# Performance work log

Measured on AMD Instinct MI355X. Metric: run time of the kernel, lower is better.

## Reference

```python
import jax, jax.numpy as jnp
import numpy as np

# hyperparams from __init__
K_SEL = 8          # SoftSelectorProxy K
R_TEMP = 1.0       # SoftSelectorProxy r (temperature)
LAM = 0.5          # SoftSelectorProxy lam (blend)
MAX_PROXY = 16     # max_proxy_points -> K_eff (N >> 16)

B, N, INPUT_DIM = 32, 16384, 64
HID, K_DIM, D_MODEL = 64, 16, 512
ANCHOR_DIM = INPUT_DIM + 2  # structural_feature_dim: x feats + saliency + normalized position


def setup_inputs() -> dict:
    key = jax.random.key(0)
    ks = jax.random.split(key, 10)
    s = lambda k, shp, fan: jax.random.normal(k, shp, jnp.float32) * (1.0 / np.sqrt(fan))
    return {
        "x": jax.random.normal(ks[0], (B, N, INPUT_DIM), jnp.float32),
        "W1": s(ks[1], (INPUT_DIM, HID), INPUT_DIM),
        "b1": jnp.zeros((HID,), jnp.float32),
        "w_e": s(ks[2], (HID,), HID),
        "w_s": s(ks[3], (HID,), HID),
        "W_lift": s(ks[4], (ANCHOR_DIM, K_DIM), ANCHOR_DIM),
        "b_lift": jnp.zeros((K_DIM,), jnp.float32),
        "W_proj": s(ks[5], (K_DIM, D_MODEL), K_DIM),
        "b_proj": jnp.zeros((D_MODEL,), jnp.float32),
        "mu": jnp.zeros((ANCHOR_DIM,), jnp.float32),
        "sigma": jnp.ones((ANCHOR_DIM,), jnp.float32),
    }


def reference(x, W1, b1, w_e, w_s, W_lift, b_lift, W_proj, b_proj, mu, sigma):
    # CausalEventModel: shared hidden, event + saliency heads
    h = jnp.tanh(jnp.einsum('bnd,dh->bnh', x, W1) + b1)          # [B,N,HID]
    saliency = jax.nn.softplus(jnp.einsum('bnh,h->bn', h, w_s))   # [B,N]
    # SoftSelectorProxy: blend of sigmoid gate and K-scaled softmax (soft top-K relaxation)
    y_star = LAM * jax.nn.sigmoid(saliency / R_TEMP) + (1.0 - LAM) * K_SEL * jax.nn.softmax(saliency / R_TEMP, axis=1)  # [B,N]
    # dense_anchor_vectors: concat features, saliency, normalized position
    pos = jnp.broadcast_to((jnp.arange(N, dtype=jnp.float32) / N)[None, :, None], (x.shape[0], N, 1))
    dense = jnp.concatenate([x, saliency[..., None], pos], axis=-1)  # [B,N,ANCHOR_DIM]
    # NormalizedLift: normalize then linear lift to k_dim
    lifted = jnp.einsum('bna,ak->bnk', (dense - mu) / sigma, W_lift) + b_lift  # [B,N,K_DIM]
    # topk selection + gather + projection
    _, top_idx = jax.lax.top_k(y_star, MAX_PROXY)                 # [B,MAX_PROXY]
    cloud = jnp.take_along_axis(lifted, top_idx[..., None], axis=1)  # [B,MAX_PROXY,K_DIM]
    tokens = jnp.einsum('bkc,cd->bkd', cloud, W_proj) + b_proj    # [B,MAX_PROXY,D_MODEL]
    return tokens, y_star
```

## Files before the change

kernel.cpp:

```cpp
#include <hip/hip_runtime.h>
#include <math.h>

#define B 32
#define N 16384
#define DIM 64
#define HID 64
#define KD 16
#define DM 512
#define MP 16

#define GRID_SAL 1024
#define ITERS 8

typedef __attribute__((ext_vector_type(8))) _Float16 f16x8;
typedef __attribute__((ext_vector_type(2))) __fp16 fph2;
typedef __attribute__((ext_vector_type(4))) float f32x4;

__device__ __forceinline__ float fast_tanh(float a) {
  const float e = __expf(2.f * a);
  return 1.f - 2.f * __builtin_amdgcn_rcpf(e + 1.f);
}

__global__ __launch_bounds__(256) void k_prepw(
    const float* __restrict__ W1, _Float16* __restrict__ Wt_hi, _Float16* __restrict__ Wt_lo) {
  const int i = blockIdx.x * 256 + threadIdx.x;
  const int col = i >> 6, k = i & 63;
  const float v = W1[k * HID + col];
  const _Float16 h = (_Float16)v;
  Wt_hi[i] = h;
  Wt_lo[i] = (_Float16)(v - (float)h);
}

__global__ __launch_bounds__(256) void k_saliency(
    const float* __restrict__ x, const _Float16* __restrict__ Wt_hi,
    const _Float16* __restrict__ Wt_lo, const float* __restrict__ b1,
    const float* __restrict__ w_s, float* __restrict__ sal) {
  const int t = threadIdx.x;
  const int lane = t & 63, wid = t >> 6;
  const int c16 = lane & 15, kq = lane >> 4;
  const int wbase = c16 * 64 + kq * 8;

  f16x8 WH[8], WL[8];
#pragma unroll
  for (int ct = 0; ct < 4; ++ct)
#pragma unroll
    for (int kc = 0; kc < 2; ++kc) {
      const int off = ct * 1024 + kc * 32 + wbase;
      WH[ct * 2 + kc] = *(const f16x8*)(Wt_hi + off);
      WL[ct * 2 + kc] = *(const f16x8*)(Wt_lo + off);
    }

#define PKSPLIT(va, vb, HW, LW) {                                                  \
    const fph2 h_ = __builtin_amdgcn_cvt_pkrtz((va), (vb));                        \
    const fph2 l_ = __builtin_amdgcn_cvt_pkrtz((va) - (float)h_[0],                \
                                               (vb) - (float)h_[1]);               \
    HW = __builtin_bit_cast(unsigned, h_);                                         \
    LW = __builtin_bit_cast(unsigned, l_); }

#define SAL_LOADS(b0, b1_, b2, b3, it_) {                                          \
    const size_t row_ = ((size_t)(it_) * GRID_SAL + blockIdx.x) * 64 + wid * 16 + c16; \
    const float* __restrict__ p_ = x + row_ * DIM + kq * 8;                        \
    b0 = *(const float4*)(p_);       b1_ = *(const float4*)(p_ + 4);               \
    b2 = *(const float4*)(p_ + 32);  b3 = *(const float4*)(p_ + 36); }

#define SAL_COMPUTE(b0, b1_, b2, b3, it_) {                                        \
    f32x4 a0 = (f32x4)0.f, a1 = (f32x4)0.f, a2 = (f32x4)0.f, a3 = (f32x4)0.f;      \
    {                                                                  \
      uint4 H, L;                                                                  \
      PKSPLIT(b0.x, b0.y, H.x, L.x); PKSPLIT(b0.z, b0.w, H.y, L.y);                \
      PKSPLIT(b1_.x, b1_.y, H.z, L.z); PKSPLIT(b1_.z, b1_.w, H.w, L.w);            \
      const f16x8 bh = __builtin_bit_cast(f16x8, H);                               \
      const f16x8 bl = __builtin_bit_cast(f16x8, L);                               \
      a0 = __builtin_amdgcn_mfma_f32_16x16x32_f16(WH[0], bh, a0, 0, 0, 0);         \
      a1 = __builtin_amdgcn_mfma_f32_16x16x32_f16(WH[2], bh, a1, 0, 0, 0);         \
      a2 = __builtin_amdgcn_mfma_f32_16x16x32_f16(WH[4], bh, a2, 0, 0, 0);         \
      a3 = __builtin_amdgcn_mfma_f32_16x16x32_f16(WH[6], bh, a3, 0, 0, 0);         \
      a0 = __builtin_amdgcn_mfma_f32_16x16x32_f16(WL[0], bh, a0, 0, 0, 0);         \
      a1 = __builtin_amdgcn_mfma_f32_16x16x32_f16(WL[2], bh, a1, 0, 0, 0);         \
      a2 = __builtin_amdgcn_mfma_f32_16x16x32_f16(WL[4], bh, a2, 0, 0, 0);         \
      a3 = __builtin_amdgcn_mfma_f32_16x16x32_f16(WL[6], bh, a3, 0, 0, 0);         \
      a0 = __builtin_amdgcn_mfma_f32_16x16x32_f16(WH[0], bl, a0, 0, 0, 0);         \
      a1 = __builtin_amdgcn_mfma_f32_16x16x32_f16(WH[2], bl, a1, 0, 0, 0);         \
      a2 = __builtin_amdgcn_mfma_f32_16x16x32_f16(WH[4], bl, a2, 0, 0, 0);         \
      a3 = __builtin_amdgcn_mfma_f32_16x16x32_f16(WH[6], bl, a3, 0, 0, 0);         \
    }                                                                              \
    {                                                                  \
      uint4 H, L;                                                                  \
      PKSPLIT(b2.x, b2.y, H.x, L.x); PKSPLIT(b2.z, b2.w, H.y, L.y);                \
      PKSPLIT(b3.x, b3.y, H.z, L.z); PKSPLIT(b3.z, b3.w, H.w, L.w);                \
      const f16x8 bh = __builtin_bit_cast(f16x8, H);                               \
      const f16x8 bl = __builtin_bit_cast(f16x8, L);                               \
      a0 = __builtin_amdgcn_mfma_f32_16x16x32_f16(WH[1], bh, a0, 0, 0, 0);         \
      a1 = __builtin_amdgcn_mfma_f32_16x16x32_f16(WH[3], bh, a1, 0, 0, 0);         \
      a2 = __builtin_amdgcn_mfma_f32_16x16x32_f16(WH[5], bh, a2, 0, 0, 0);         \
      a3 = __builtin_amdgcn_mfma_f32_16x16x32_f16(WH[7], bh, a3, 0, 0, 0);         \
      a0 = __builtin_amdgcn_mfma_f32_16x16x32_f16(WL[1], bh, a0, 0, 0, 0);         \
      a1 = __builtin_amdgcn_mfma_f32_16x16x32_f16(WL[3], bh, a1, 0, 0, 0);         \
      a2 = __builtin_amdgcn_mfma_f32_16x16x32_f16(WL[5], bh, a2, 0, 0, 0);         \
      a3 = __builtin_amdgcn_mfma_f32_16x16x32_f16(WL[7], bh, a3, 0, 0, 0);         \
      a0 = __builtin_amdgcn_mfma_f32_16x16x32_f16(WH[1], bl, a0, 0, 0, 0);         \
      a1 = __builtin_amdgcn_mfma_f32_16x16x32_f16(WH[3], bl, a1, 0, 0, 0);         \
      a2 = __builtin_amdgcn_mfma_f32_16x16x32_f16(WH[5], bl, a2, 0, 0, 0);         \
      a3 = __builtin_amdgcn_mfma_f32_16x16x32_f16(WH[7], bl, a3, 0, 0, 0);         \
    }                                                                              \
       \
    float s = 0.f;                                                                 \
    { const f32x4 wv = *(const f32x4*)(w_s + kq * 4);                              \
      const f32x4 bv = *(const f32x4*)(b1 + kq * 4);                               \
      s = fmaf(wv[0], fast_tanh(a0[0] + bv[0]), s);                                \
      s = fmaf(wv[1], fast_tanh(a0[1] + bv[1]), s);                                \
      s = fmaf(wv[2], fast_tanh(a0[2] + bv[2]), s);                                \
      s = fmaf(wv[3], fast_tanh(a0[3] + bv[3]), s); }                              \
    { const f32x4 wv = *(const f32x4*)(w_s + 16 + kq * 4);                         \
      const f32x4 bv = *(const f32x4*)(b1 + 16 + kq * 4);                          \
      s = fmaf(wv[0], fast_tanh(a1[0] + bv[0]), s);                                \
      s = fmaf(wv[1], fast_tanh(a1[1] + bv[1]), s);                                \
      s = fmaf(wv[2], fast_tanh(a1[2] + bv[2]), s);                                \
      s = fmaf(wv[3], fast_tanh(a1[3] + bv[3]), s); }                              \
    { const f32x4 wv = *(const f32x4*)(w_s + 32 + kq * 4);                         \
      const f32x4 bv = *(const f32x4*)(b1 + 32 + kq * 4);                          \
      s = fmaf(wv[0], fast_tanh(a2[0] + bv[0]), s);                                \
      s = fmaf(wv[1], fast_tanh(a2[1] + bv[1]), s);                                \
      s = fmaf(wv[2], fast_tanh(a2[2] + bv[2]), s);                                \
      s = fmaf(wv[3], fast_tanh(a2[3] + bv[3]), s); }                              \
    { const f32x4 wv = *(const f32x4*)(w_s + 48 + kq * 4);                         \
      const f32x4 bv = *(const f32x4*)(b1 + 48 + kq * 4);                          \
      s = fmaf(wv[0], fast_tanh(a3[0] + bv[0]), s);                                \
      s = fmaf(wv[1], fast_tanh(a3[1] + bv[1]), s);                                \
      s = fmaf(wv[2], fast_tanh(a3[2] + bv[2]), s);                                \
      s = fmaf(wv[3], fast_tanh(a3[3] + bv[3]), s); }                              \
    s += __shfl_xor(s, 16);                                                        \
    s += __shfl_xor(s, 32);                                                        \
    if (lane < 16) {                                                               \
      const size_t sr_ = ((size_t)(it_) * GRID_SAL + blockIdx.x) * 64 + wid * 16 + lane; \
      const float z_ = __expf(-fabsf(s));                                          \
      sal[sr_] = fmaxf(s, 0.f) + __logf(1.f + z_);          \
    } }

  float4 pA0, pA1, pA2, pA3;
  float4 pB0, pB1, pB2, pB3;

  SAL_LOADS(pA0, pA1, pA2, pA3, 0);
#pragma unroll 1
  for (int it2 = 0; it2 < ITERS; it2 += 2) {
    SAL_LOADS(pB0, pB1, pB2, pB3, it2 + 1);
    SAL_COMPUTE(pA0, pA1, pA2, pA3, it2);
    if (it2 + 2 < ITERS) SAL_LOADS(pA0, pA1, pA2, pA3, it2 + 2);
    SAL_COMPUTE(pB0, pB1, pB2, pB3, it2 + 1);
  }
#undef SAL_LOADS
#undef SAL_COMPUTE
#undef PKSPLIT
}

__global__ __launch_bounds__(256) void k_chunk(
    const float* __restrict__ sal, float* __restrict__ cmax, float* __restrict__ csum,
    float* __restrict__ cval, int* __restrict__ cidx) {
  __shared__ float sb[4], ss[4], wv[4];
  __shared__ int wi[4];
  const int t = threadIdx.x, c = blockIdx.x;
  const int rowoff = (c & 7) * 2048;
  const size_t gbase = (size_t)c * 2048;
  float v[8];
#pragma unroll
  for (int j = 0; j < 8; ++j) v[j] = sal[gbase + t + 256 * j];

  float m = v[0];
#pragma unroll
  for (int j = 1; j < 8; ++j) m = fmaxf(m, v[j]);
#pragma unroll
  for (int off = 1; off < 64; off <<= 1) m = fmaxf(m, __shfl_xor(m, off));
  if ((t & 63) == 0) sb[t >> 6] = m;
  __syncthreads();
  m = fmaxf(fmaxf(sb[0], sb[1]), fmaxf(sb[2], sb[3]));

  float se = 0.f;
#pragma unroll
  for (int j = 0; j < 8; ++j) se += __expf(v[j] - m);
#pragma unroll
  for (int off = 1; off < 64; off <<= 1) se += __shfl_xor(se, off);
  if ((t & 63) == 0) ss[t >> 6] = se;
  __syncthreads();
  if (t == 0) { cmax[c] = m; csum[c] = ss[0] + ss[1] + ss[2] + ss[3]; }

  for (int k = 0; k < MP; ++k) {
    float bv = v[0]; int bj = 0;
#pragma unroll
    for (int j = 1; j < 8; ++j)
      if (v[j] > bv) { bv = v[j]; bj = j; }
    int bi = rowoff + t + 256 * bj;
#pragma unroll
    for (int off = 1; off < 64; off <<= 1) {
      const float ov = __shfl_xor(bv, off);
      const int   oi = __shfl_xor(bi, off);
      if (ov > bv || (ov == bv && oi < bi)) { bv = ov; bi = oi; }
    }
    if ((t & 63) == 0) { wv[t >> 6] = bv; wi[t >> 6] = bi; }
    __syncthreads();
    float Bv = wv[0]; int Bi = wi[0];
#pragma unroll
    for (int w = 1; w < 4; ++w)
      if (wv[w] > Bv || (wv[w] == Bv && wi[w] < Bi)) { Bv = wv[w]; Bi = wi[w]; }
    if (t == 0) { cval[c * MP + k] = Bv; cidx[c * MP + k] = Bi; }
    const int relidx = Bi - rowoff;
#pragma unroll
    for (int jj = 0; jj < 8; ++jj)
      if (relidx == t + 256 * jj) v[jj] = -INFINITY;
    __syncthreads();
  }
}

__global__ __launch_bounds__(256) void k_ystar(
    float* __restrict__ y, const float* __restrict__ cmax, const float* __restrict__ csum) {
  const int b = blockIdx.x >> 6;
  const int gi = blockIdx.x * 256 + threadIdx.x;
  float mx = cmax[b * 8];
#pragma unroll
  for (int c = 1; c < 8; ++c) mx = fmaxf(mx, cmax[b * 8 + c]);
  float S = 0.f;
#pragma unroll
  for (int c = 0; c < 8; ++c) S += csum[b * 8 + c] * __expf(cmax[b * 8 + c] - mx);
  const float inv = __builtin_amdgcn_rcpf(S);
  const float v = y[gi];
  const float sig = __builtin_amdgcn_rcpf(1.f + __expf(-v));
  y[gi] = fmaf(0.5f, sig, 4.f * __expf(v - mx) * inv);
}

__global__ __launch_bounds__(256) void k_toptokens(
    const float* __restrict__ cval, const int* __restrict__ cidx,
    const float* __restrict__ x,
    const float* __restrict__ W_lift, const float* __restrict__ b_lift,
    const float* __restrict__ W_proj, const float* __restrict__ b_proj,
    const float* __restrict__ mu, const float* __restrict__ sigma,
    float* __restrict__ tokens) {
  __shared__ float wv[4];
  __shared__ int wi[4];
  __shared__ float s_val[MP];
  __shared__ int s_idx[MP];
  __shared__ float lifted[MP][KD + 1];
  const int b = blockIdx.x, t = threadIdx.x;

  float v = -INFINITY; int i = 0x7fffffff;
  if (t < 128) { v = cval[b * 128 + t]; i = cidx[b * 128 + t]; }
  for (int k = 0; k < MP; ++k) {
    float bv = v; int bi = i;
#pragma unroll
    for (int off = 1; off < 64; off <<= 1) {
      const float ov = __shfl_xor(bv, off);
      const int   oi = __shfl_xor(bi, off);
      if (ov > bv || (ov == bv && oi < bi)) { bv = ov; bi = oi; }
    }
    if ((t & 63) == 0) { wv[t >> 6] = bv; wi[t >> 6] = bi; }
    __syncthreads();
    float Bv = wv[0]; int Bi = wi[0];
#pragma unroll
    for (int w = 1; w < 4; ++w)
      if (wv[w] > Bv || (wv[w] == Bv && wi[w] < Bi)) { Bv = wv[w]; Bi = wi[w]; }
    if (t == 0) { s_val[k] = Bv; s_idx[k] = Bi; }
    if (i == Bi) v = -INFINITY;
    __syncthreads();
  }

  const int p = t >> 4, kd = t & 15;
  const int idx = s_idx[p];
  const float salv = s_val[p];
  const float* __restrict__ xr = x + ((size_t)b * N + idx) * DIM;
  float a = b_lift[kd];
#pragma unroll 8
  for (int d = 0; d < DIM; ++d)
    a = fmaf((xr[d] - mu[d]) * __builtin_amdgcn_rcpf(sigma[d]), W_lift[d * KD + kd], a);
  a = fmaf((salv - mu[64]) * __builtin_amdgcn_rcpf(sigma[64]), W_lift[64 * KD + kd], a);
  a = fmaf(((float)idx / (float)N - mu[65]) * __builtin_amdgcn_rcpf(sigma[65]),
           W_lift[65 * KD + kd], a);
  lifted[p][kd] = a;
  __syncthreads();

  const float2* __restrict__ Wp2 = (const float2*)W_proj;
  const float2 bp = ((const float2*)b_proj)[t];
#pragma unroll 1
  for (int p2 = 0; p2 < MP; ++p2) {
    float2 o = bp;
#pragma unroll
    for (int c = 0; c < KD; ++c) {
      const float2 w = Wp2[c * 256 + t];
      o.x = fmaf(lifted[p2][c], w.x, o.x);
      o.y = fmaf(lifted[p2][c], w.y, o.y);
    }
    ((float2*)(tokens + ((size_t)b * MP + p2) * DM))[t] = o;
  }
}

extern "C" void kernel_launch(void* const* d_in, const int* in_sizes, int n_in,
                              void* d_out, int out_size, void* d_ws, size_t ws_size,
                              hipStream_t stream) {
  const float* x      = (const float*)d_in[0];
  const float* W1     = (const float*)d_in[1];
  const float* b1     = (const float*)d_in[2];
  const float* w_s    = (const float*)d_in[4];
  const float* W_lift = (const float*)d_in[5];
  const float* b_lift = (const float*)d_in[6];
  const float* W_proj = (const float*)d_in[7];
  const float* b_proj = (const float*)d_in[8];
  const float* mu     = (const float*)d_in[9];
  const float* sigma  = (const float*)d_in[10];

  float* tokens = (float*)d_out;
  float* ystar  = (float*)d_out + (size_t)B * MP * DM;

  float* cmax    = (float*)d_ws + 1024;
  float* csum    = (float*)d_ws + 1280;
  float* cval    = (float*)d_ws + 1600;
  int*   cidx    = (int*)d_ws + 5696;
  _Float16* Wt_hi = (_Float16*)((float*)d_ws + 9792);
  _Float16* Wt_lo = Wt_hi + 4096;

  k_prepw<<<16, 256, 0, stream>>>(W1, Wt_hi, Wt_lo);
  k_saliency<<<GRID_SAL, 256, 0, stream>>>(x, Wt_hi, Wt_lo, b1, w_s, ystar);
  k_chunk<<<(B * N) / 2048, 256, 0, stream>>>(ystar, cmax, csum, cval, cidx);
  k_ystar<<<(B * N) / 256, 256, 0, stream>>>(ystar, cmax, csum);
  k_toptokens<<<B, 256, 0, stream>>>(cval, cidx, x, W_lift, b_lift,
                                     W_proj, b_proj, mu, sigma, tokens);
}
```

Measured before the change: 81.85 us.

## Fuse chunk softmax, y_star and top-k token kernels into one per-row kernel

Replaces the three post-saliency kernels (chunked max/sum/top-16, y_star normalization, cross-chunk merge plus lift/projection) with a single 1024-thread block per batch row. That block computes the row softmax stats, writes y_star, selects the top 16 and produces the tokens. This removes two launches and the workspace round trips for partial results. The trade-off is that only 32 blocks run this stage, so parallelism is low, with 16 serial block-wide top-k rounds over 16 waves. The saliency kernel grid is also doubled with half the iterations per block.

Result: slower. 103.2 us (+26.0%).

```diff
diff --git a/kernel.cpp b/kernel.cpp
--- a/kernel.cpp
+++ b/kernel.cpp
@@ -9,8 +9,8 @@
 #define DM 512
 #define MP 16
 
-#define GRID_SAL 1024
-#define ITERS 8
+#define GRID_SAL 2048
+#define ITERS 4
 
 typedef __attribute__((ext_vector_type(8))) _Float16 f16x8;
 typedef __attribute__((ext_vector_type(2))) __fp16 fph2;
@@ -103,7 +103,6 @@
       a2 = __builtin_amdgcn_mfma_f32_16x16x32_f16(WH[5], bl, a2, 0, 0, 0);         \
       a3 = __builtin_amdgcn_mfma_f32_16x16x32_f16(WH[7], bl, a3, 0, 0, 0);         \
     }                                                                              \
-       \
     float s = 0.f;                                                                 \
     { const f32x4 wv = *(const f32x4*)(w_s + kq * 4);                              \
       const f32x4 bv = *(const f32x4*)(b1 + kq * 4);                               \
@@ -153,140 +152,112 @@
 #undef PKSPLIT
 }
 
-__global__ __launch_bounds__(256) void k_chunk(
-    const float* __restrict__ sal, float* __restrict__ cmax, float* __restrict__ csum,
-    float* __restrict__ cval, int* __restrict__ cidx) {
-  __shared__ float sb[4], ss[4], wv[4];
-  __shared__ int wi[4];
-  const int t = threadIdx.x, c = blockIdx.x;
-  const int rowoff = (c & 7) * 2048;
-  const size_t gbase = (size_t)c * 2048;
-  float v[8];
-#pragma unroll
-  for (int j = 0; j < 8; ++j) v[j] = sal[gbase + t + 256 * j];
+__global__ __launch_bounds__(1024) void k_rowtok(
+    float* __restrict__ y,
+    const float* __restrict__ x,
+    const float* __restrict__ W_lift, const float* __restrict__ b_lift,
+    const float* __restrict__ W_proj, const float* __restrict__ b_proj,
+    const float* __restrict__ mu, const float* __restrict__ sigma,
+    float* __restrict__ tokens) {
+  __shared__ float sb[16], ss[16], wvs[16];
+  __shared__ int wis[16];
+  __shared__ float s_val[MP];
+  __shared__ int s_idx[MP];
+  __shared__ float lifted[MP][KD + 1];
+  const int b = blockIdx.x, t = threadIdx.x;
+  const int wid = t >> 6, lane = t & 63;
+  float* __restrict__ row = y + (size_t)b * N;
+
+  float v[16];
+#pragma unroll
+  for (int j = 0; j < 16; ++j) v[j] = row[t + 1024 * j];
 
   float m = v[0];
 #pragma unroll
-  for (int j = 1; j < 8; ++j) m = fmaxf(m, v[j]);
+  for (int j = 1; j < 16; ++j) m = fmaxf(m, v[j]);
 #pragma unroll
   for (int off = 1; off < 64; off <<= 1) m = fmaxf(m, __shfl_xor(m, off));
-  if ((t & 63) == 0) sb[t >> 6] = m;
+  if (lane == 0) sb[wid] = m;
   __syncthreads();
-  m = fmaxf(fmaxf(sb[0], sb[1]), fmaxf(sb[2], sb[3]));
+  m = sb[0];
+#pragma unroll
+  for (int w = 1; w < 16; ++w) m = fmaxf(m, sb[w]);
 
   float se = 0.f;
 #pragma unroll
-  for (int j = 0; j < 8; ++j) se += __expf(v[j] - m);
+  for (int j = 0; j < 16; ++j) se += __expf(v[j] - m);
 #pragma unroll
   for (int off = 1; off < 64; off <<= 1) se += __shfl_xor(se, off);
-  if ((t & 63) == 0) ss[t >> 6] = se;
+  if (lane == 0) ss[wid] = se;
   __syncthreads();
-  if (t == 0) { cmax[c] = m; csum[c] = ss[0] + ss[1] + ss[2] + ss[3]; }
+  float S = ss[0];
+#pragma unroll
+  for (int w = 1; w < 16; ++w) S += ss[w];
+  const float inv = __builtin_amdgcn_rcpf(S);
+
+#pragma unroll
+  for (int j = 0; j < 16; ++j) {
+    const float sv = v[j];
+    const float sig = __builtin_amdgcn_rcpf(1.f + __expf(-sv));
+    row[t + 1024 * j] = fmaf(0.5f, sig, 4.f * __expf(sv - m) * inv);
+  }
 
   for (int k = 0; k < MP; ++k) {
     float bv = v[0]; int bj = 0;
 #pragma unroll
-    for (int j = 1; j < 8; ++j)
+    for (int j = 1; j < 16; ++j)
       if (v[j] > bv) { bv = v[j]; bj = j; }
-    int bi = rowoff + t + 256 * bj;
+    int bi = t + 1024 * bj;
 #pragma unroll
     for (int off = 1; off < 64; off <<= 1) {
       const float ov = __shfl_xor(bv, off);
       const int   oi = __shfl_xor(bi, off);
       if (ov > bv || (ov == bv && oi < bi)) { bv = ov; bi = oi; }
     }
-    if ((t & 63) == 0) { wv[t >> 6] = bv; wi[t >> 6] = bi; }
+    if (lane == 0) { wvs[wid] = bv; wis[wid] = bi; }
     __syncthreads();
-    float Bv = wv[0]; int Bi = wi[0];
-#pragma unroll
-    for (int w = 1; w < 4; ++w)
-      if (wv[w] > Bv || (wv[w] == Bv && wi[w] < Bi)) { Bv = wv[w]; Bi = wi[w]; }
-    if (t == 0) { cval[c * MP + k] = Bv; cidx[c * MP + k] = Bi; }
-    const int relidx = Bi - rowoff;
-#pragma unroll
-    for (int jj = 0; jj < 8; ++jj)
-      if (relidx == t + 256 * jj) v[jj] = -INFINITY;
+    float Bv = wvs[0]; int Bi = wis[0];
+#pragma unroll
+    for (int w = 1; w < 16; ++w)
+      if (wvs[w] > Bv || (wvs[w] == Bv && wis[w] < Bi)) { Bv = wvs[w]; Bi = wis[w]; }
+    if (t == 0) { s_val[k] = Bv; s_idx[k] = Bi; }
+    const int rel = Bi - t;
+#pragma unroll
+    for (int jj = 0; jj < 16; ++jj)
+      if (rel == 1024 * jj) v[jj] = -INFINITY;
     __syncthreads();
   }
-}
-
-__global__ __launch_bounds__(256) void k_ystar(
-    float* __restrict__ y, const float* __restrict__ cmax, const float* __restrict__ csum) {
-  const int b = blockIdx.x >> 6;
-  const int gi = blockIdx.x * 256 + threadIdx.x;
-  float mx = cmax[b * 8];
-#pragma unroll
-  for (int c = 1; c < 8; ++c) mx = fmaxf(mx, cmax[b * 8 + c]);
-  float S = 0.f;
-#pragma unroll
-  for (int c = 0; c < 8; ++c) S += csum[b * 8 + c] * __expf(cmax[b * 8 + c] - mx);
-  const float inv = __builtin_amdgcn_rcpf(S);
-  const float v = y[gi];
-  const float sig = __builtin_amdgcn_rcpf(1.f + __expf(-v));
-  y[gi] = fmaf(0.5f, sig, 4.f * __expf(v - mx) * inv);
-}
-
-__global__ __launch_bounds__(256) void k_toptokens(
-    const float* __restrict__ cval, const int* __restrict__ cidx,
-    const float* __restrict__ x,
-    const float* __restrict__ W_lift, const float* __restrict__ b_lift,
-    const float* __restrict__ W_proj, const float* __restrict__ b_proj,
-    const float* __restrict__ mu, const float* __restrict__ sigma,
-    float* __restrict__ tokens) {
-  __shared__ float wv[4];
-  __shared__ int wi[4];
-  __shared__ float s_val[MP];
-  __shared__ int s_idx[MP];
-  __shared__ float lifted[MP][KD + 1];
-  const int b = blockIdx.x, t = threadIdx.x;
-
-  float v = -INFINITY; int i = 0x7fffffff;
-  if (t < 128) { v = cval[b * 128 + t]; i = cidx[b * 128 + t]; }
-  for (int k = 0; k < MP; ++k) {
-    float bv = v; int bi = i;
-#pragma unroll
-    for (int off = 1; off < 64; off <<= 1) {
-      const float ov = __shfl_xor(bv, off);
-      const int   oi = __shfl_xor(bi, off);
-      if (ov > bv || (ov == bv && oi < bi)) { bv = ov; bi = oi; }
-    }
-    if ((t & 63) == 0) { wv[t >> 6] = bv; wi[t >> 6] = bi; }
-    __syncthreads();
-    float Bv = wv[0]; int Bi = wi[0];
-#pragma unroll
-    for (int w = 1; w < 4; ++w)
-      if (wv[w] > Bv || (wv[w] == Bv && wi[w] < Bi)) { Bv = wv[w]; Bi = wi[w]; }
-    if (t == 0) { s_val[k] = Bv; s_idx[k] = Bi; }
-    if (i == Bi) v = -INFINITY;
-    __syncthreads();
-  }
-
-  const int p = t >> 4, kd = t & 15;
-  const int idx = s_idx[p];
-  const float salv = s_val[p];
-  const float* __restrict__ xr = x + ((size_t)b * N + idx) * DIM;
-  float a = b_lift[kd];
+
+  if (t < 256) {
+    const int p = t >> 4, kd = t & 15;
+    const int idx = s_idx[p];
+    const float salv = s_val[p];
+    const float* __restrict__ xr = x + ((size_t)b * N + idx) * DIM;
+    float a = b_lift[kd];
 #pragma unroll 8
-  for (int d = 0; d < DIM; ++d)
-    a = fmaf((xr[d] - mu[d]) * __builtin_amdgcn_rcpf(sigma[d]), W_lift[d * KD + kd], a);
-  a = fmaf((salv - mu[64]) * __builtin_amdgcn_rcpf(sigma[64]), W_lift[64 * KD + kd], a);
-  a = fmaf(((float)idx / (float)N - mu[65]) * __builtin_amdgcn_rcpf(sigma[65]),
-           W_lift[65 * KD + kd], a);
-  lifted[p][kd] = a;
+    for (int d = 0; d < DIM; ++d)
+      a = fmaf((xr[d] - mu[d]) * __builtin_amdgcn_rcpf(sigma[d]), W_lift[d * KD + kd], a);
+    a = fmaf((salv - mu[64]) * __builtin_amdgcn_rcpf(sigma[64]), W_lift[64 * KD + kd], a);
+    a = fmaf(((float)idx * (1.f / (float)N) - mu[65]) * __builtin_amdgcn_rcpf(sigma[65]),
+             W_lift[65 * KD + kd], a);
+    lifted[p][kd] = a;
+  }
   __syncthreads();
 
+  const int d2 = t & 255, pg = t >> 8;
   const float2* __restrict__ Wp2 = (const float2*)W_proj;
-  const float2 bp = ((const float2*)b_proj)[t];
-#pragma unroll 1
-  for (int p2 = 0; p2 < MP; ++p2) {
+  const float2 bp = ((const float2*)b_proj)[d2];
+#pragma unroll
+  for (int q = 0; q < 4; ++q) {
+    const int p2 = pg * 4 + q;
     float2 o = bp;
 #pragma unroll
     for (int c = 0; c < KD; ++c) {
-      const float2 w = Wp2[c * 256 + t];
+      const float2 w = Wp2[c * 256 + d2];
       o.x = fmaf(lifted[p2][c], w.x, o.x);
       o.y = fmaf(lifted[p2][c], w.y, o.y);
     }
-    ((float2*)(tokens + ((size_t)b * MP + p2) * DM))[t] = o;
+    ((float2*)(tokens + ((size_t)b * MP + p2) * DM))[d2] = o;
   }
 }
 
@@ -307,17 +278,11 @@
   float* tokens = (float*)d_out;
   float* ystar  = (float*)d_out + (size_t)B * MP * DM;
 
-  float* cmax    = (float*)d_ws + 1024;
-  float* csum    = (float*)d_ws + 1280;
-  float* cval    = (float*)d_ws + 1600;
-  int*   cidx    = (int*)d_ws + 5696;
-  _Float16* Wt_hi = (_Float16*)((float*)d_ws + 9792);
+  _Float16* Wt_hi = (_Float16*)d_ws;
   _Float16* Wt_lo = Wt_hi + 4096;
 
   k_prepw<<<16, 256, 0, stream>>>(W1, Wt_hi, Wt_lo);
   k_saliency<<<GRID_SAL, 256, 0, stream>>>(x, Wt_hi, Wt_lo, b1, w_s, ystar);
-  k_chunk<<<(B * N) / 2048, 256, 0, stream>>>(ystar, cmax, csum, cval, cidx);
-  k_ystar<<<(B * N) / 256, 256, 0, stream>>>(ystar, cmax, csum);
-  k_toptokens<<<B, 256, 0, stream>>>(cval, cidx, x, W_lift, b_lift,
-                                     W_proj, b_proj, mu, sigma, tokens);
-}
+  k_rowtok<<<B, 1024, 0, stream>>>(ystar, x, W_lift, b_lift,
+                                   W_proj, b_proj, mu, sigma, tokens);
+}
```

## Fold weight prep into saliency kernel and merge ystar with top-token kernel

Applied to the files above, without the earlier changes.

Removes the separate W1 transpose/split kernel: each saliency block now loads W1, splits it into fp16 hi/lo, and transposes it into padded shared memory before loading its MFMA fragments. The y_star normalisation and the top-K token projection are merged into one launch, with the first 32 blocks doing tokens and the rest doing elementwise y_star. This cuts two kernel launches and their gaps, at the cost of redundant W1 conversion in every one of the 1024 saliency blocks plus extra LDS use and a barrier.

Result: faster. 69.49 us, median of 2 (-15.1%).

```diff
diff --git a/kernel.cpp b/kernel.cpp
--- a/kernel.cpp
+++ b/kernel.cpp
@@ -21,33 +21,35 @@
   return 1.f - 2.f * __builtin_amdgcn_rcpf(e + 1.f);
 }
 
-__global__ __launch_bounds__(256) void k_prepw(
-    const float* __restrict__ W1, _Float16* __restrict__ Wt_hi, _Float16* __restrict__ Wt_lo) {
-  const int i = blockIdx.x * 256 + threadIdx.x;
-  const int col = i >> 6, k = i & 63;
-  const float v = W1[k * HID + col];
-  const _Float16 h = (_Float16)v;
-  Wt_hi[i] = h;
-  Wt_lo[i] = (_Float16)(v - (float)h);
-}
-
 __global__ __launch_bounds__(256) void k_saliency(
-    const float* __restrict__ x, const _Float16* __restrict__ Wt_hi,
-    const _Float16* __restrict__ Wt_lo, const float* __restrict__ b1,
-    const float* __restrict__ w_s, float* __restrict__ sal) {
+    const float* __restrict__ x, const float* __restrict__ W1,
+    const float* __restrict__ b1, const float* __restrict__ w_s,
+    float* __restrict__ sal) {
   const int t = threadIdx.x;
   const int lane = t & 63, wid = t >> 6;
   const int c16 = lane & 15, kq = lane >> 4;
-  const int wbase = c16 * 64 + kq * 8;
+
+  __shared__ __align__(16) _Float16 lWh[64 * 72];
+  __shared__ __align__(16) _Float16 lWl[64 * 72];
+#pragma unroll
+  for (int j = 0; j < 16; ++j) {
+    const int i = t + 256 * j;
+    const int k = i >> 6, col = i & 63;
+    const float v = W1[i];
+    const _Float16 h = (_Float16)v;
+    lWh[col * 72 + k] = h;
+    lWl[col * 72 + k] = (_Float16)(v - (float)h);
+  }
+  __syncthreads();
 
   f16x8 WH[8], WL[8];
 #pragma unroll
   for (int ct = 0; ct < 4; ++ct)
 #pragma unroll
     for (int kc = 0; kc < 2; ++kc) {
-      const int off = ct * 1024 + kc * 32 + wbase;
-      WH[ct * 2 + kc] = *(const f16x8*)(Wt_hi + off);
-      WL[ct * 2 + kc] = *(const f16x8*)(Wt_lo + off);
+      const int off = (ct * 16 + c16) * 72 + kc * 32 + kq * 8;
+      WH[ct * 2 + kc] = *(const f16x8*)(lWh + off);
+      WL[ct * 2 + kc] = *(const f16x8*)(lWl + off);
     }
 
 #define PKSPLIT(va, vb, HW, LW) {                                                  \
@@ -103,7 +105,6 @@
       a2 = __builtin_amdgcn_mfma_f32_16x16x32_f16(WH[5], bl, a2, 0, 0, 0);         \
       a3 = __builtin_amdgcn_mfma_f32_16x16x32_f16(WH[7], bl, a3, 0, 0, 0);         \
     }                                                                              \
-       \
     float s = 0.f;                                                                 \
     { const f32x4 wv = *(const f32x4*)(w_s + kq * 4);                              \
       const f32x4 bv = *(const f32x4*)(b1 + kq * 4);                               \
@@ -210,35 +211,39 @@
   }
 }
 
-__global__ __launch_bounds__(256) void k_ystar(
-    float* __restrict__ y, const float* __restrict__ cmax, const float* __restrict__ csum) {
-  const int b = blockIdx.x >> 6;
-  const int gi = blockIdx.x * 256 + threadIdx.x;
-  float mx = cmax[b * 8];
-#pragma unroll
-  for (int c = 1; c < 8; ++c) mx = fmaxf(mx, cmax[b * 8 + c]);
-  float S = 0.f;
-#pragma unroll
-  for (int c = 0; c < 8; ++c) S += csum[b * 8 + c] * __expf(cmax[b * 8 + c] - mx);
-  const float inv = __builtin_amdgcn_rcpf(S);
-  const float v = y[gi];
-  const float sig = __builtin_amdgcn_rcpf(1.f + __expf(-v));
-  y[gi] = fmaf(0.5f, sig, 4.f * __expf(v - mx) * inv);
-}
-
-__global__ __launch_bounds__(256) void k_toptokens(
+__global__ __launch_bounds__(256) void k_final(
+    float* __restrict__ y, const float* __restrict__ cmax, const float* __restrict__ csum,
     const float* __restrict__ cval, const int* __restrict__ cidx,
     const float* __restrict__ x,
     const float* __restrict__ W_lift, const float* __restrict__ b_lift,
     const float* __restrict__ W_proj, const float* __restrict__ b_proj,
     const float* __restrict__ mu, const float* __restrict__ sigma,
     float* __restrict__ tokens) {
+  const int t = threadIdx.x;
+
+  if (blockIdx.x >= 32) {
+    const int bid = blockIdx.x - 32;
+    const int b = bid >> 6;
+    const int gi = bid * 256 + t;
+    float mx = cmax[b * 8];
+#pragma unroll
+    for (int c = 1; c < 8; ++c) mx = fmaxf(mx, cmax[b * 8 + c]);
+    float S = 0.f;
+#pragma unroll
+    for (int c = 0; c < 8; ++c) S += csum[b * 8 + c] * __expf(cmax[b * 8 + c] - mx);
+    const float inv = __builtin_amdgcn_rcpf(S);
+    const float v = y[gi];
+    const float sig = __builtin_amdgcn_rcpf(1.f + __expf(-v));
+    y[gi] = fmaf(0.5f, sig, 4.f * __expf(v - mx) * inv);
+    return;
+  }
+
   __shared__ float wv[4];
   __shared__ int wi[4];
   __shared__ float s_val[MP];
   __shared__ int s_idx[MP];
   __shared__ float lifted[MP][KD + 1];
-  const int b = blockIdx.x, t = threadIdx.x;
+  const int b = blockIdx.x;
 
   float v = -INFINITY; int i = 0x7fffffff;
   if (t < 128) { v = cval[b * 128 + t]; i = cidx[b * 128 + t]; }
@@ -311,13 +316,10 @@
   float* csum    = (float*)d_ws + 1280;
   float* cval    = (float*)d_ws + 1600;
   int*   cidx    = (int*)d_ws + 5696;
-  _Float16* Wt_hi = (_Float16*)((float*)d_ws + 9792);
-  _Float16* Wt_lo = Wt_hi + 4096;
-
-  k_prepw<<<16, 256, 0, stream>>>(W1, Wt_hi, Wt_lo);
-  k_saliency<<<GRID_SAL, 256, 0, stream>>>(x, Wt_hi, Wt_lo, b1, w_s, ystar);
+
+  k_saliency<<<GRID_SAL, 256, 0, stream>>>(x, W1, b1, w_s, ystar);
   k_chunk<<<(B * N) / 2048, 256, 0, stream>>>(ystar, cmax, csum, cval, cidx);
-  k_ystar<<<(B * N) / 256, 256, 0, stream>>>(ystar, cmax, csum);
-  k_toptokens<<<B, 256, 0, stream>>>(cval, cidx, x, W_lift, b_lift,
-                                     W_proj, b_proj, mu, sigma, tokens);
-}
+  k_final<<<2048 + 32, 256, 0, stream>>>(ystar, cmax, csum, cval, cidx, x,
+                                         W_lift, b_lift, W_proj, b_proj,
+                                         mu, sigma, tokens);
+}
```
